# Kernel tuning notes

Hardware: AMD Instinct MI355X
Metric: run time of the kernel (lower is better)

Reference implementation:

```python
import jax, jax.numpy as jnp
import numpy as np

RING_WORLD_SIZE = 4  # number of ring steps / KV sequence chunks


def _ring_flash_attention(q, k, v, ring_size):
    # q,k,v: [B, S, H, D]; non-causal full attention computed blockwise over
    # KV chunks (one per ring step) with numerically-stable online LSE merge,
    # mirroring _compact_ring_fwd + update_out_and_lse.
    B, S, H, D = q.shape
    scale = D ** (-0.5)
    chunk = S // ring_size
    out = None  # [B, S, H, D] accumulated in fp32
    lse = None  # [B, H, S] running log-sum-exp
    for step in range(ring_size):
        k_blk = jax.lax.dynamic_slice_in_dim(k, step * chunk, chunk, axis=1)
        v_blk = jax.lax.dynamic_slice_in_dim(v, step * chunk, chunk, axis=1)
        # scores: [B, H, Sq, Sk_blk]
        scores = jnp.einsum('bqhd,bkhd->bhqk', q, k_blk) * scale
        block_lse = jax.scipy.special.logsumexp(scores, axis=-1)  # [B,H,Sq]
        probs = jnp.exp(scores - block_lse[..., None])
        block_out = jnp.einsum('bhqk,bkhd->bqhd', probs, v_blk)
        if out is None:
            out, lse = block_out, block_lse
        else:
            new_lse = jnp.logaddexp(lse, block_lse)
            w_old = jnp.exp(lse - new_lse)       # [B,H,Sq]
            w_new = jnp.exp(block_lse - new_lse)
            # broadcast weights to [B,Sq,H,1]
            out = (jnp.transpose(w_old, (0, 2, 1))[..., None] * out
                   + jnp.transpose(w_new, (0, 2, 1))[..., None] * block_out)
            lse = new_lse
    return out.astype(q.dtype)


def setup_inputs() -> dict:
    key = jax.random.key(0)
    kq, kk, kv = jax.random.split(key, 3)
    shape = (1, 4096, 16, 128)
    return {
        'query': jax.random.normal(kq, shape, dtype=jnp.float32),
        'key': jax.random.normal(kk, shape, dtype=jnp.float32),
        'value': jax.random.normal(kv, shape, dtype=jnp.float32),
    }


def reference(query, key, value):
    # Ulysses all-to-all is identity on a single logical device; the ring loop
    # with lossless (error-feedback) KV compression reduces to blockwise
    # attention with online softmax merging.
    return _ring_flash_attention(query, key, value, RING_WORLD_SIZE)
```

## Files before the change

kernel.cpp:

```cpp
#include <hip/hip_runtime.h>
#include <hip/hip_bf16.h>

#define S_LEN 4096
#define NH    16
#define DD    128
#define HD    2048
#define QB    64
#define KB    64
#define NT    (S_LEN/KB)

typedef __bf16 bf16_t;
typedef bf16_t bf16x8 __attribute__((ext_vector_type(8)));
typedef float  f32x4  __attribute__((ext_vector_type(4)));

static __device__ __forceinline__ bf16x8 pack8(float4 a, float4 b, float s) {
  bf16x8 v;
  v[0]=(bf16_t)(a.x*s); v[1]=(bf16_t)(a.y*s); v[2]=(bf16_t)(a.z*s); v[3]=(bf16_t)(a.w*s);
  v[4]=(bf16_t)(b.x*s); v[5]=(bf16_t)(b.y*s); v[6]=(bf16_t)(b.z*s); v[7]=(bf16_t)(b.w*s);
  return v;
}

static __device__ __forceinline__ void gload_lds16(const void* g, void* l) {
  __builtin_amdgcn_global_load_lds((const __attribute__((address_space(1))) void*)g,
                                   (__attribute__((address_space(3))) void*)l, 16, 0, 0);
}

__global__ __launch_bounds__(256) void prep_k(const float* __restrict__ Kg,
                                              bf16_t* __restrict__ Kp) {
  const int kt = blockIdx.x, h = blockIdx.y, tid = threadIdx.x;
  __shared__ bf16_t tile[KB][DD + 8];
  #pragma unroll
  for (int it = 0; it < 8; ++it) {
    int lin4 = it*256 + tid;
    int r  = lin4 >> 5;
    int dc = (lin4 & 31) * 4;
    float4 a = *(const float4*)(Kg + (size_t)(kt*KB + r)*HD + h*DD + dc);
    tile[r][dc+0]=(bf16_t)a.x; tile[r][dc+1]=(bf16_t)a.y;
    tile[r][dc+2]=(bf16_t)a.z; tile[r][dc+3]=(bf16_t)a.w;
  }
  __syncthreads();
  bf16_t* out = Kp + (size_t)(h*NT + kt)*8192;
  #pragma unroll
  for (int it = 0; it < 4; ++it) {
    int cid = it*256 + tid;
    int f = cid >> 6, l = cid & 63;
    int b = f >> 2, c = f & 3;
    int row = b*16 + (l & 15);
    int d0  = c*32 + (l >> 4)*8;
    bf16x8 v = *(const bf16x8*)(&tile[row][d0]);
    *(bf16x8*)(out + (size_t)cid*8) = v;
  }
}

__global__ __launch_bounds__(256) void prep_v(const float* __restrict__ Vg,
                                              bf16_t* __restrict__ Vp) {
  const int kt = blockIdx.x, h = blockIdx.y, tid = threadIdx.x;
  __shared__ bf16_t tile[KB][DD + 8];
  #pragma unroll
  for (int it = 0; it < 8; ++it) {
    int lin4 = it*256 + tid;
    int r  = lin4 >> 5;
    int dc = (lin4 & 31) * 4;
    float4 a = *(const float4*)(Vg + (size_t)(kt*KB + r)*HD + h*DD + dc);
    tile[r][dc+0]=(bf16_t)a.x; tile[r][dc+1]=(bf16_t)a.y;
    tile[r][dc+2]=(bf16_t)a.z; tile[r][dc+3]=(bf16_t)a.w;
  }
  __syncthreads();
  bf16_t* out = Vp + (size_t)(h*NT + kt)*8192;
  #pragma unroll
  for (int it = 0; it < 4; ++it) {
    int cid = it*256 + tid;
    int f = cid >> 6, l = cid & 63;
    int ks = f >> 3, db = f & 7;
    int d  = db*16 + (l & 15);
    int c0 = ks*32 + (l >> 4)*8;
    bf16x8 v;
    #pragma unroll
    for (int m = 0; m < 8; ++m) {
      int c = c0 + m;
      int k = 32*(c>>5) + 16*((c>>2)&1) + 4*((c>>3)&3) + (c&3);
      v[m] = tile[k][d];
    }
    *(bf16x8*)(out + (size_t)cid*8) = v;
  }
}

__global__ __launch_bounds__(128, 2) void attn_fwd(const float* __restrict__ Qg,
                                                   const bf16_t* __restrict__ Kp,
                                                   const bf16_t* __restrict__ Vp,
                                                   float* __restrict__ Og) {
  const int phys = blockIdx.x;
  const int logical = (phys & 7) * 128 + (phys >> 3);
  const int h  = logical >> 6;
  const int qt = logical & 63;
  const int tid  = threadIdx.x;
  const int wid  = tid >> 6;
  const int lane = tid & 63;
  const int l16  = lane & 15;
  const int lg   = lane >> 4;
  const int lo16 = lane * 16;

  __shared__ alignas(16) bf16_t Vt[2][8192];

  const float qs = 0.08838834764831845f * 1.4426950408889634f;
  bf16x8 qf[2][4];
  #pragma unroll
  for (int g = 0; g < 2; ++g) {
    const int qrow = qt*QB + wid*32 + g*16 + l16;
    const float* qp = Qg + (size_t)qrow*HD + h*DD + lg*8;
    #pragma unroll
    for (int c = 0; c < 4; ++c) {
      float4 a = *(const float4*)(qp + c*32);
      float4 b = *(const float4*)(qp + c*32 + 4);
      qf[g][c] = pack8(a, b, qs);
    }
  }
  bf16x8 onesf;
  #pragma unroll
  for (int j = 0; j < 8; ++j) onesf[j] = (bf16_t)1.0f;
  asm volatile("" ::: "memory");

  const char* KpH = (const char*)(Kp + (size_t)h*NT*8192);
  bf16x8 kreg[16];
  auto issue_k = [&](int kt) {
    const char* kg = KpH + (size_t)kt*16384 + lo16;
    #pragma unroll
    for (int f = 0; f < 16; ++f) kreg[f] = *(const bf16x8*)(kg + (f << 10));
  };

  const int lo = tid*16;
  const char* VpH = (const char*)(Vp + (size_t)h*NT*8192);
  auto issue_v = [&](int kt) {
    const char* vg = VpH + (size_t)kt*16384 + lo;
    char* vl = (char*)&Vt[kt & 1][0] + lo;
    #pragma unroll
    for (int p = 0; p < 8; ++p) gload_lds16(vg + p*2048, vl + p*2048);
  };

  f32x4 acc[2][8];
  f32x4 acc_l[2];
  #pragma unroll
  for (int g = 0; g < 2; ++g) {
    #pragma unroll
    for (int i = 0; i < 8; ++i) acc[g][i] = (f32x4){0.f,0.f,0.f,0.f};
    acc_l[g] = (f32x4){0.f,0.f,0.f,0.f};
  }
  float m_run[2] = {-__builtin_inff(), -__builtin_inff()};

  issue_v(0);
  issue_v(1);
  issue_k(0);
  asm volatile("s_waitcnt vmcnt(24)" ::: "memory");
  __builtin_amdgcn_s_barrier();

  for (int kt = 0; kt < NT; ++kt) {
    const int cur = kt & 1;

    f32x4 sc[2][4];
    #pragma unroll
    for (int g = 0; g < 2; ++g)
      #pragma unroll
      for (int b = 0; b < 4; ++b) sc[g][b] = (f32x4){0.f,0.f,0.f,0.f};
    __builtin_amdgcn_s_setprio(1);
    #pragma unroll
    for (int b = 0; b < 4; ++b) {
      #pragma unroll
      for (int c = 0; c < 4; ++c) {
        bf16x8 kb = kreg[b*4 + c];
        sc[0][b] = __builtin_amdgcn_mfma_f32_16x16x32_bf16(kb, qf[0][c], sc[0][b], 0, 0, 0);
        sc[1][b] = __builtin_amdgcn_mfma_f32_16x16x32_bf16(kb, qf[1][c], sc[1][b], 0, 0, 0);
      }
    }
    __builtin_amdgcn_s_setprio(0);

    if (kt + 1 < NT) issue_k(kt + 1);

    bf16x8 pp[2][2];
    #pragma unroll
    for (int g = 0; g < 2; ++g) {
      float pmax;
      {
        float a0 = fmaxf(fmaxf(sc[g][0][0], sc[g][0][1]), sc[g][0][2]);
        float a1 = fmaxf(fmaxf(sc[g][0][3], sc[g][1][0]), sc[g][1][1]);
        float a2 = fmaxf(fmaxf(sc[g][1][2], sc[g][1][3]), sc[g][2][0]);
        float a3 = fmaxf(fmaxf(sc[g][2][1], sc[g][2][2]), sc[g][2][3]);
        float a4 = fmaxf(fmaxf(sc[g][3][0], sc[g][3][1]), sc[g][3][2]);
        float b0 = fmaxf(fmaxf(a0, a1), a2);
        float b1 = fmaxf(fmaxf(a3, a4), sc[g][3][3]);
        pmax = fmaxf(b0, b1);
        pmax = fmaxf(pmax, __shfl_xor(pmax, 16));
        pmax = fmaxf(pmax, __shfl_xor(pmax, 32));
      }
      if (!__all(pmax - m_run[g] <= 8.0f)) {
        float mnew  = fmaxf(m_run[g], pmax);
        float alpha = exp2f(m_run[g] - mnew);
        m_run[g] = mnew;
        #pragma unroll
        for (int i = 0; i < 8; ++i) {
          #pragma unroll
          for (int r = 0; r < 4; ++r) acc[g][i][r] *= alpha;
        }
        #pragma unroll
        for (int r = 0; r < 4; ++r) acc_l[g][r] *= alpha;
      }
      #pragma unroll
      for (int b = 0; b < 4; ++b) {
        #pragma unroll
        for (int r = 0; r < 4; ++r) {
          float p = exp2f(sc[g][b][r] - m_run[g]);
          pp[g][b >> 1][(b & 1)*4 + r] = (bf16_t)p;
        }
      }
    }

    {
      const char* VtB = (const char*)&Vt[cur][0] + lo16;
      __builtin_amdgcn_s_setprio(1);
      #pragma unroll
      for (int ks = 0; ks < 2; ++ks) {
        acc_l[0] = __builtin_amdgcn_mfma_f32_16x16x32_bf16(onesf, pp[0][ks], acc_l[0], 0, 0, 0);
        acc_l[1] = __builtin_amdgcn_mfma_f32_16x16x32_bf16(onesf, pp[1][ks], acc_l[1], 0, 0, 0);
        #pragma unroll
        for (int db = 0; db < 8; ++db) {
          bf16x8 va = *(const bf16x8*)(VtB + ((ks*8 + db) << 10));
          acc[0][db] = __builtin_amdgcn_mfma_f32_16x16x32_bf16(va, pp[0][ks], acc[0][db], 0, 0, 0);
          acc[1][db] = __builtin_amdgcn_mfma_f32_16x16x32_bf16(va, pp[1][ks], acc[1][db], 0, 0, 0);
        }
      }
      __builtin_amdgcn_s_setprio(0);
    }

    asm volatile("s_waitcnt lgkmcnt(0)" ::: "memory");
    if (kt + 1 < NT) {
      asm volatile("s_waitcnt vmcnt(16)" ::: "memory");
    }
    __builtin_amdgcn_sched_barrier(0);
    __builtin_amdgcn_s_barrier();
    if (kt + 2 < NT) issue_v(kt + 2);
  }

  #pragma unroll
  for (int g = 0; g < 2; ++g) {
    const int qrow = qt*QB + wid*32 + g*16 + l16;
    const float inv = 1.0f / acc_l[g][0];
    float* op = Og + (size_t)qrow*HD + h*DD + lg*4;
    #pragma unroll
    for (int db = 0; db < 8; ++db) {
      float4 o;
      o.x = acc[g][db][0]*inv; o.y = acc[g][db][1]*inv;
      o.z = acc[g][db][2]*inv; o.w = acc[g][db][3]*inv;
      *(float4*)(op + db*16) = o;
    }
  }
}

extern "C" void kernel_launch(void* const* d_in, const int* in_sizes, int n_in,
                              void* d_out, int out_size, void* d_ws, size_t ws_size,
                              hipStream_t stream) {
  const float* Q = (const float*)d_in[0];
  const float* K = (const float*)d_in[1];
  const float* V = (const float*)d_in[2];
  float* O = (float*)d_out;
  bf16_t* Kp = (bf16_t*)d_ws;
  bf16_t* Vp = Kp + (size_t)NH*S_LEN*DD;
  prep_k<<<dim3(NT, NH), 256, 0, stream>>>(K, Kp);
  prep_v<<<dim3(NT, NH), 256, 0, stream>>>(V, Vp);
  attn_fwd<<<dim3(1024), 128, 0, stream>>>(Q, Kp, Vp, O);
}
```

Before: 203.3 us.

## Load V tiles directly from global into registers instead of LDS double-buffer

Drops the LDS double buffer for V, along with the async global-to-LDS loads and the per-iteration barrier. Each wave now loads its V fragments straight from global memory into registers, with the first half issued right after the QK MFMAs and the second half after the softmax. This removes LDS traffic and block-wide synchronisation. The cost is that both waves now fetch the same V data separately, V prefetch depth drops to within one iteration so global latency is more exposed, and register pressure rises.

```diff
diff --git a/kernel.cpp b/kernel.cpp
--- a/kernel.cpp
+++ b/kernel.cpp
@@ -18,11 +18,6 @@
   v[0]=(bf16_t)(a.x*s); v[1]=(bf16_t)(a.y*s); v[2]=(bf16_t)(a.z*s); v[3]=(bf16_t)(a.w*s);
   v[4]=(bf16_t)(b.x*s); v[5]=(bf16_t)(b.y*s); v[6]=(bf16_t)(b.z*s); v[7]=(bf16_t)(b.w*s);
   return v;
-}
-
-static __device__ __forceinline__ void gload_lds16(const void* g, void* l) {
-  __builtin_amdgcn_global_load_lds((const __attribute__((address_space(1))) void*)g,
-                                   (__attribute__((address_space(3))) void*)l, 16, 0, 0);
 }
 
 __global__ __launch_bounds__(256) void prep_k(const float* __restrict__ Kg,
@@ -100,8 +95,6 @@
   const int lg   = lane >> 4;
   const int lo16 = lane * 16;
 
-  __shared__ alignas(16) bf16_t Vt[2][8192];
-
   const float qs = 0.08838834764831845f * 1.4426950408889634f;
   bf16x8 qf[2][4];
   #pragma unroll
@@ -118,24 +111,13 @@
   bf16x8 onesf;
   #pragma unroll
   for (int j = 0; j < 8; ++j) onesf[j] = (bf16_t)1.0f;
-  asm volatile("" ::: "memory");
-
-  const char* KpH = (const char*)(Kp + (size_t)h*NT*8192);
+
+  const char* KpH = (const char*)(Kp + (size_t)h*NT*8192) + lo16;
+  const char* VpH = (const char*)(Vp + (size_t)h*NT*8192) + lo16;
+
   bf16x8 kreg[16];
-  auto issue_k = [&](int kt) {
-    const char* kg = KpH + (size_t)kt*16384 + lo16;
-    #pragma unroll
-    for (int f = 0; f < 16; ++f) kreg[f] = *(const bf16x8*)(kg + (f << 10));
-  };
-
-  const int lo = tid*16;
-  const char* VpH = (const char*)(Vp + (size_t)h*NT*8192);
-  auto issue_v = [&](int kt) {
-    const char* vg = VpH + (size_t)kt*16384 + lo;
-    char* vl = (char*)&Vt[kt & 1][0] + lo;
-    #pragma unroll
-    for (int p = 0; p < 8; ++p) gload_lds16(vg + p*2048, vl + p*2048);
-  };
+  #pragma unroll
+  for (int f = 0; f < 16; ++f) kreg[f] = *(const bf16x8*)(KpH + (f << 10));
 
   f32x4 acc[2][8];
   f32x4 acc_l[2];
@@ -147,15 +129,7 @@
   }
   float m_run[2] = {-__builtin_inff(), -__builtin_inff()};
 
-  issue_v(0);
-  issue_v(1);
-  issue_k(0);
-  asm volatile("s_waitcnt vmcnt(24)" ::: "memory");
-  __builtin_amdgcn_s_barrier();
-
   for (int kt = 0; kt < NT; ++kt) {
-    const int cur = kt & 1;
-
     f32x4 sc[2][4];
     #pragma unroll
     for (int g = 0; g < 2; ++g)
@@ -173,7 +147,16 @@
     }
     __builtin_amdgcn_s_setprio(0);
 
-    if (kt + 1 < NT) issue_k(kt + 1);
+    const char* vt = VpH + (size_t)kt*16384;
+    bf16x8 va0[8];
+    #pragma unroll
+    for (int f = 0; f < 8; ++f) va0[f] = *(const bf16x8*)(vt + (f << 10));
+
+    if (kt + 1 < NT) {
+      const char* kg = KpH + (size_t)(kt + 1)*16384;
+      #pragma unroll
+      for (int f = 0; f < 16; ++f) kreg[f] = *(const bf16x8*)(kg + (f << 10));
+    }
 
     bf16x8 pp[2][2];
     #pragma unroll
@@ -213,30 +196,26 @@
       }
     }
 
-    {
-      const char* VtB = (const char*)&Vt[cur][0] + lo16;
-      __builtin_amdgcn_s_setprio(1);
-      #pragma unroll
-      for (int ks = 0; ks < 2; ++ks) {
-        acc_l[0] = __builtin_amdgcn_mfma_f32_16x16x32_bf16(onesf, pp[0][ks], acc_l[0], 0, 0, 0);
-        acc_l[1] = __builtin_amdgcn_mfma_f32_16x16x32_bf16(onesf, pp[1][ks], acc_l[1], 0, 0, 0);
-        #pragma unroll
-        for (int db = 0; db < 8; ++db) {
-          bf16x8 va = *(const bf16x8*)(VtB + ((ks*8 + db) << 10));
-          acc[0][db] = __builtin_amdgcn_mfma_f32_16x16x32_bf16(va, pp[0][ks], acc[0][db], 0, 0, 0);
-          acc[1][db] = __builtin_amdgcn_mfma_f32_16x16x32_bf16(va, pp[1][ks], acc[1][db], 0, 0, 0);
-        }
-      }
-      __builtin_amdgcn_s_setprio(0);
-    }
-
-    asm volatile("s_waitcnt lgkmcnt(0)" ::: "memory");
-    if (kt + 1 < NT) {
-      asm volatile("s_waitcnt vmcnt(16)" ::: "memory");
-    }
-    __builtin_amdgcn_sched_barrier(0);
-    __builtin_amdgcn_s_barrier();
-    if (kt + 2 < NT) issue_v(kt + 2);
+    bf16x8 va1[8];
+    #pragma unroll
+    for (int f = 0; f < 8; ++f) va1[f] = *(const bf16x8*)(vt + ((8 + f) << 10));
+
+    __builtin_amdgcn_s_setprio(1);
+    acc_l[0] = __builtin_amdgcn_mfma_f32_16x16x32_bf16(onesf, pp[0][0], acc_l[0], 0, 0, 0);
+    acc_l[1] = __builtin_amdgcn_mfma_f32_16x16x32_bf16(onesf, pp[1][0], acc_l[1], 0, 0, 0);
+    #pragma unroll
+    for (int db = 0; db < 8; ++db) {
+      acc[0][db] = __builtin_amdgcn_mfma_f32_16x16x32_bf16(va0[db], pp[0][0], acc[0][db], 0, 0, 0);
+      acc[1][db] = __builtin_amdgcn_mfma_f32_16x16x32_bf16(va0[db], pp[1][0], acc[1][db], 0, 0, 0);
+    }
+    acc_l[0] = __builtin_amdgcn_mfma_f32_16x16x32_bf16(onesf, pp[0][1], acc_l[0], 0, 0, 0);
+    acc_l[1] = __builtin_amdgcn_mfma_f32_16x16x32_bf16(onesf, pp[1][1], acc_l[1], 0, 0, 0);
+    #pragma unroll
+    for (int db = 0; db < 8; ++db) {
+      acc[0][db] = __builtin_amdgcn_mfma_f32_16x16x32_bf16(va1[db], pp[0][1], acc[0][db], 0, 0, 0);
+      acc[1][db] = __builtin_amdgcn_mfma_f32_16x16x32_bf16(va1[db], pp[1][1], acc[1][db], 0, 0, 0);
+    }
+    __builtin_amdgcn_s_setprio(0);
   }
 
   #pragma unroll
```

Result: no change. 200.5 us (-1.4%).
